# Optimization experiments

Measured on AMD Instinct MI355X. Metric: run time of the kernel, lower is better.

Reference implementation:

```python
import jax, jax.numpy as jnp
import numpy as np

B, T, D = 2, 2048, 1024
H = 16
HD = D // H  # 64


def setup_inputs() -> dict:
    key = jax.random.key(0)
    k1, k2, k3, k4, k5 = jax.random.split(key, 5)
    s = 0.02
    return {
        "x": jax.random.normal(k1, (B, T, D), dtype=jnp.float32),
        "Wqkv": jax.random.normal(k2, (D, 3 * D), dtype=jnp.float32) * s,
        "bqkv": jax.random.normal(k3, (3 * D,), dtype=jnp.float32) * s,
        "Wout": jax.random.normal(k4, (D, D), dtype=jnp.float32) * s,
        "bout": jax.random.normal(k5, (D,), dtype=jnp.float32) * s,
    }


def reference(x, Wqkv, bqkv, Wout, bout):
    b, t, c = x.shape
    qkv = (x @ Wqkv + bqkv).reshape(b, t, 3, H, HD)
    q = jnp.transpose(qkv[:, :, 0], (0, 2, 1, 3))  # [B,H,T,HD]
    k = jnp.transpose(qkv[:, :, 1], (0, 2, 1, 3))
    v = jnp.transpose(qkv[:, :, 2], (0, 2, 1, 3))
    att = jnp.einsum("bhqd,bhkd->bhqk", q, k) * (HD ** -0.5)
    mask = jnp.tril(jnp.ones((t, t), dtype=bool))  # causal, no past kv
    att = jnp.where(mask, att, -jnp.inf)
    att = jax.nn.softmax(att, axis=-1)
    y = jnp.einsum("bhqk,bhkd->bhqd", att, v)
    y = jnp.transpose(y, (0, 2, 1, 3)).reshape(b, t, c)
    return y @ Wout + bout
```

## Files before the change

### kernel.cpp

```cpp
#include <hip/hip_runtime.h>
#include <hip/hip_bf16.h>
#include <math.h>

#define B_  2
#define T_  2048
#define D_  1024
#define H_  16
#define HD_ 64

typedef __attribute__((ext_vector_type(8))) short short8;
typedef __attribute__((ext_vector_type(4))) float f32x4;

#if __has_builtin(__builtin_amdgcn_exp2f)
#define EXP2F __builtin_amdgcn_exp2f
#else
#define EXP2F exp2f
#endif

__device__ __forceinline__ ushort f2bf(float x) {
    unsigned u = __builtin_bit_cast(unsigned, x);
    return (ushort)((u + 0x7FFFu + ((u >> 16) & 1u)) >> 16);
}

__device__ __forceinline__ unsigned pack_bf2_fast(float a, float b) {
    unsigned ua = __builtin_bit_cast(unsigned, a) + 0x8000u;
    unsigned ub = __builtin_bit_cast(unsigned, b) + 0x8000u;
    return (ua >> 16) | (ub & 0xFFFF0000u);
}

__device__ __forceinline__ void load_lds_16B(const ushort* g, ushort* l) {
    __builtin_amdgcn_global_load_lds(
        (const __attribute__((address_space(1))) unsigned*)g,
        (__attribute__((address_space(3))) unsigned*)l, 16, 0, 0);
}

__global__ __launch_bounds__(256)
void cast_x_kernel(const float* __restrict__ x, ushort* __restrict__ xb, int n4)
{
    int i = blockIdx.x * blockDim.x + threadIdx.x;
    for (; i < n4; i += gridDim.x * blockDim.x) {
        float4 v = ((const float4*)x)[i];
        ushort4 o = { f2bf(v.x), f2bf(v.y), f2bf(v.z), f2bf(v.w) };
        ((ushort4*)xb)[i] = o;
    }
}

__global__ __launch_bounds__(256)
void transpose_cast_w(const float* __restrict__ W, ushort* __restrict__ Wt,
                      int K, int M)
{
    __shared__ ushort Ts[64][65];
    const int m0 = blockIdx.x * 64, k0 = blockIdx.y * 64;
    const int tr = threadIdx.x >> 4;
    const int tc = threadIdx.x & 15;
    #pragma unroll
    for (int it = 0; it < 4; it++) {
        int k = tr + it * 16;
        float4 v = *(const float4*)&W[(size_t)(k0 + k) * M + m0 + tc * 4];
        Ts[tc * 4 + 0][k] = f2bf(v.x);
        Ts[tc * 4 + 1][k] = f2bf(v.y);
        Ts[tc * 4 + 2][k] = f2bf(v.z);
        Ts[tc * 4 + 3][k] = f2bf(v.w);
    }
    __syncthreads();
    const int mr = threadIdx.x >> 2;
    const int c4 = threadIdx.x & 3;
    #pragma unroll
    for (int it = 0; it < 4; it++) {
        int kk = c4 * 16 + it * 4;
        ushort4 o = { Ts[mr][kk], Ts[mr][kk + 1], Ts[mr][kk + 2], Ts[mr][kk + 3] };
        *(ushort4*)&Wt[(size_t)(m0 + mr) * K + k0 + kk] = o;
    }
}

template<int MODE>
__global__ __launch_bounds__(256)
void mfma_gemm(const ushort* __restrict__ A, const ushort* __restrict__ Bt,
               const float* __restrict__ bias, float* __restrict__ C,
               ushort* __restrict__ Qg, ushort* __restrict__ Kg,
               ushort* __restrict__ Vtg, int K, int M)
{
    __shared__ __align__(16) ushort lds[16384];
    ushort* Asl = lds;
    ushort* Bsl = lds + 8192;

    const int tid = threadIdx.x;
    const int w  = tid >> 6, L = tid & 63;
    const int lt = L & 15, lq = L >> 4;
    const int wr = w >> 1, wc = w & 1;
    const int m0 = blockIdx.x * 128, n0 = blockIdx.y * 128;
    const int rsub = L >> 3;
    const int pgr  = L & 7;

    f32x4 acc[4][4] = {};

    for (int k0 = 0; k0 < K; k0 += 64) {
        __syncthreads();
        #pragma unroll
        for (int j = 0; j < 4; j++) {
            const int row  = (w * 4 + j) * 8 + rsub;
            const int gran = pgr ^ rsub;
            load_lds_16B(A  + (size_t)(n0 + row) * K + k0 + gran * 8,
                         &Asl[row * 64 + pgr * 8]);
            load_lds_16B(Bt + (size_t)(m0 + row) * K + k0 + gran * 8,
                         &Bsl[row * 64 + pgr * 8]);
        }
        __syncthreads();

        #pragma unroll
        for (int ks = 0; ks < 2; ks++) {
            short8 af[4], bf[4];
            #pragma unroll
            for (int i = 0; i < 4; i++) {
                const int ra = wr * 64 + i * 16 + lt;
                af[i] = *(const short8*)&Asl[ra * 64 + (((ks * 4 + lq) ^ (ra & 7)) * 8)];
                const int rb = wc * 64 + i * 16 + lt;
                bf[i] = *(const short8*)&Bsl[rb * 64 + (((ks * 4 + lq) ^ (rb & 7)) * 8)];
            }
            #pragma unroll
            for (int i = 0; i < 4; i++)
                #pragma unroll
                for (int j = 0; j < 4; j++)
                    acc[i][j] = __builtin_amdgcn_mfma_f32_16x16x32_bf16(af[i], bf[j], acc[i][j], 0, 0, 0);
        }
    }

    if (MODE == 0) {
        #pragma unroll
        for (int j = 0; j < 4; j++) {
            const int m = m0 + wc * 64 + j * 16 + lt;
            const float bv = bias[m];
            #pragma unroll
            for (int i = 0; i < 4; i++) {
                const int n = n0 + wr * 64 + i * 16 + lq * 4;
                #pragma unroll
                for (int r = 0; r < 4; r++)
                    C[(size_t)(n + r) * M + m] = acc[i][j][r] + bv;
            }
        }
    } else {
        const int s = m0 >> 10;
        const float qs = (s == 0) ? 0.18033688011112042f : 1.0f;
        #pragma unroll
        for (int j = 0; j < 4; j++) {
            const int m = m0 + wc * 64 + j * 16 + lt;
            const float bv = bias[m];
            const int h = (m >> 6) & 15, d = m & 63;
            #pragma unroll
            for (int i = 0; i < 4; i++) {
                const int n = n0 + wr * 64 + i * 16 + lq * 4;
                const int b = n >> 11, t = n & 2047;
                if (s < 2) {
                    ushort* dst = (s == 0 ? Qg : Kg);
                    #pragma unroll
                    for (int r = 0; r < 4; r++)
                        dst[((size_t)(b * H_ + h) * T_ + t + r) * HD_ + d] =
                            f2bf((acc[i][j][r] + bv) * qs);
                } else {
                    ushort4 o = { f2bf(acc[i][j][0] + bv), f2bf(acc[i][j][1] + bv),
                                  f2bf(acc[i][j][2] + bv), f2bf(acc[i][j][3] + bv) };
                    *(ushort4*)&Vtg[((size_t)(b * H_ + h) * HD_ + d) * T_ + t] = o;
                }
            }
        }
    }
}

__global__ __launch_bounds__(256, 4)
void attn_mfma(const ushort* __restrict__ Qg, const ushort* __restrict__ Kg,
               const ushort* __restrict__ Vtg, ushort* __restrict__ yb)
{
    const int h = blockIdx.y, b = blockIdx.z;
    const int flip = ((blockIdx.y >> 3) ^ blockIdx.z) & 1;
    const int qb = flip ? blockIdx.x : (31 - blockIdx.x);
    const int tid = threadIdx.x;
    const int w  = tid >> 6, L = tid & 63;
    const int lt = L & 15, lq = L >> 4;
    const int kswz = lt & 7;

    __shared__ __align__(16) ushort Ks [128 * 64];
    __shared__ __align__(16) ushort Vts[64 * 128];
    __shared__ __align__(16) ushort Ps [4][16 * 40];

    const size_t bh = (size_t)(b * H_ + h);
    const ushort* Qbase  = Qg  + bh * T_ * HD_;
    const ushort* Kbase  = Kg  + bh * T_ * HD_;
    const ushort* Vtbase = Vtg + bh * HD_ * T_;

    const int q_glob = qb * 64 + w * 16 + lt;
    const short8 qf0 = *(const short8*)(Qbase + (size_t)q_glob * HD_ + lq * 8);
    const short8 qf1 = *(const short8*)(Qbase + (size_t)q_glob * HD_ + 32 + lq * 8);

    f32x4 acc_o[4] = {};
    float lsum = 0.f;

    const int krow = tid >> 3, kpg = tid & 7;
    const int vrow = tid >> 4, vpg = tid & 15;
    const int nk = (qb + 2) >> 1;

    for (int kb = 0; kb < nk; kb++) {
        __syncthreads();
        #pragma unroll
        for (int rr = 0; rr < 4; rr++) {
            const int row = krow + 32 * rr;
            load_lds_16B(Kbase + (size_t)(kb * 128 + row) * HD_ + (kpg ^ (row & 7)) * 8,
                         &Ks[row * 64 + kpg * 8]);
        }
        #pragma unroll
        for (int rr = 0; rr < 4; rr++) {
            const int d = vrow + 16 * rr;
            load_lds_16B(Vtbase + (size_t)d * T_ + kb * 128 + (vpg ^ (d & 7)) * 8,
                         &Vts[d * 128 + vpg * 8]);
        }
        __syncthreads();

        if (kb < nk - 1) {
            #pragma unroll
            for (int ks = 0; ks < 4; ks++) {
                const int row0 = (2 * ks) * 16 + lt;
                const int row1 = row0 + 16;
                short8 a00 = *(const short8*)&Ks[row0 * 64 + ((lq ^ kswz) * 8)];
                short8 a01 = *(const short8*)&Ks[row0 * 64 + (((4 + lq) ^ kswz) * 8)];
                short8 a10 = *(const short8*)&Ks[row1 * 64 + ((lq ^ kswz) * 8)];
                short8 a11 = *(const short8*)&Ks[row1 * 64 + (((4 + lq) ^ kswz) * 8)];
                f32x4 c0 = {}, c1 = {};
                c0 = __builtin_amdgcn_mfma_f32_16x16x32_bf16(a00, qf0, c0, 0, 0, 0);
                c0 = __builtin_amdgcn_mfma_f32_16x16x32_bf16(a01, qf1, c0, 0, 0, 0);
                c1 = __builtin_amdgcn_mfma_f32_16x16x32_bf16(a10, qf0, c1, 0, 0, 0);
                c1 = __builtin_amdgcn_mfma_f32_16x16x32_bf16(a11, qf1, c1, 0, 0, 0);

                float p0 = EXP2F(c0[0]), p1 = EXP2F(c0[1]);
                float p2 = EXP2F(c0[2]), p3 = EXP2F(c0[3]);
                float p4 = EXP2F(c1[0]), p5 = EXP2F(c1[1]);
                float p6 = EXP2F(c1[2]), p7 = EXP2F(c1[3]);
                lsum += ((p0 + p1) + (p2 + p3)) + ((p4 + p5) + (p6 + p7));
                uint2 pk0 = { pack_bf2_fast(p0, p1), pack_bf2_fast(p2, p3) };
                uint2 pk1 = { pack_bf2_fast(p4, p5), pack_bf2_fast(p6, p7) };
                *(uint2*)&Ps[w][lt * 40 + lq * 4]      = pk0;
                *(uint2*)&Ps[w][lt * 40 + 16 + lq * 4] = pk1;

                short8 pf = *(const short8*)&Ps[w][lt * 40 + lq * 8];

                #pragma unroll
                for (int dt = 0; dt < 4; dt++) {
                    const int vr = dt * 16 + lt;
                    short8 vf = *(const short8*)&Vts[vr * 128 + (((ks * 4 + lq) ^ kswz) * 8)];
                    acc_o[dt] = __builtin_amdgcn_mfma_f32_16x16x32_bf16(pf, vf, acc_o[dt], 0, 0, 0);
                }
            }
        } else {
            const int ksN = (qb & 1) ? 4 : 2;
            const int mk0 = (qb & 1) ? 2 : 0;
            for (int ks = 0; ks < ksN; ks++) {
                const int row0 = (2 * ks) * 16 + lt;
                const int row1 = row0 + 16;
                short8 a00 = *(const short8*)&Ks[row0 * 64 + ((lq ^ kswz) * 8)];
                short8 a01 = *(const short8*)&Ks[row0 * 64 + (((4 + lq) ^ kswz) * 8)];
                short8 a10 = *(const short8*)&Ks[row1 * 64 + ((lq ^ kswz) * 8)];
                short8 a11 = *(const short8*)&Ks[row1 * 64 + (((4 + lq) ^ kswz) * 8)];
                f32x4 c0 = {}, c1 = {};
                c0 = __builtin_amdgcn_mfma_f32_16x16x32_bf16(a00, qf0, c0, 0, 0, 0);
                c0 = __builtin_amdgcn_mfma_f32_16x16x32_bf16(a01, qf1, c0, 0, 0, 0);
                c1 = __builtin_amdgcn_mfma_f32_16x16x32_bf16(a10, qf0, c1, 0, 0, 0);
                c1 = __builtin_amdgcn_mfma_f32_16x16x32_bf16(a11, qf1, c1, 0, 0, 0);

                float p[8];
                #pragma unroll
                for (int r = 0; r < 4; r++) { p[r] = EXP2F(c0[r]); p[4 + r] = EXP2F(c1[r]); }
                if (ks >= mk0) {
                    const int key0 = kb * 128 + (2 * ks) * 16 + lq * 4;
                    #pragma unroll
                    for (int r = 0; r < 4; r++) {
                        if (key0 + r > q_glob)      p[r] = 0.f;
                        if (key0 + 16 + r > q_glob) p[4 + r] = 0.f;
                    }
                }
                lsum += ((p[0] + p[1]) + (p[2] + p[3])) + ((p[4] + p[5]) + (p[6] + p[7]));
                uint2 pk0 = { pack_bf2_fast(p[0], p[1]), pack_bf2_fast(p[2], p[3]) };
                uint2 pk1 = { pack_bf2_fast(p[4], p[5]), pack_bf2_fast(p[6], p[7]) };
                *(uint2*)&Ps[w][lt * 40 + lq * 4]      = pk0;
                *(uint2*)&Ps[w][lt * 40 + 16 + lq * 4] = pk1;

                short8 pf = *(const short8*)&Ps[w][lt * 40 + lq * 8];

                #pragma unroll
                for (int dt = 0; dt < 4; dt++) {
                    const int vr = dt * 16 + lt;
                    short8 vf = *(const short8*)&Vts[vr * 128 + (((ks * 4 + lq) ^ kswz) * 8)];
                    acc_o[dt] = __builtin_amdgcn_mfma_f32_16x16x32_bf16(pf, vf, acc_o[dt], 0, 0, 0);
                }
            }
        }
    }

    lsum += __shfl_xor(lsum, 16, 64);
    lsum += __shfl_xor(lsum, 32, 64);
    const float inv = 1.0f / lsum;

    float linv[4];
    #pragma unroll
    for (int r = 0; r < 4; r++) linv[r] = __shfl(inv, lq * 4 + r, 64);

    ushort* ybase = yb + (size_t)(b * T_ + qb * 64 + w * 16) * D_ + h * HD_;
    #pragma unroll
    for (int r = 0; r < 4; r++)
        #pragma unroll
        for (int dt = 0; dt < 4; dt++)
            ybase[(size_t)(lq * 4 + r) * D_ + dt * 16 + lt] = f2bf(acc_o[dt][r] * linv[r]);
}

extern "C" void kernel_launch(void* const* d_in, const int* in_sizes, int n_in,
                              void* d_out, int out_size, void* d_ws, size_t ws_size,
                              hipStream_t stream)
{
    const float* x    = (const float*)d_in[0];
    const float* Wqkv = (const float*)d_in[1];
    const float* bqkv = (const float*)d_in[2];
    const float* Wout = (const float*)d_in[3];
    const float* bout = (const float*)d_in[4];
    float* out = (float*)d_out;

    char* ws = (char*)d_ws;
    const size_t NT = (size_t)B_ * T_;
    ushort* xb     = (ushort*)ws;
    ushort* Wqkvt  = (ushort*)(ws + NT * D_ * 2);
    ushort* Woutt  = (ushort*)(ws + NT * D_ * 2 + (size_t)3 * D_ * D_ * 2);
    char*   p      = ws + NT * D_ * 2 + (size_t)4 * D_ * D_ * 2;
    const size_t qkv_elems = (size_t)B_ * H_ * T_ * HD_;
    ushort* Qg  = (ushort*)p;
    ushort* Kg  = (ushort*)(p + qkv_elems * 2);
    ushort* Vtg = (ushort*)(p + qkv_elems * 4);
    ushort* yb  = (ushort*)(p + qkv_elems * 6);

    cast_x_kernel<<<1024, 256, 0, stream>>>(x, xb, (int)(NT * D_ / 4));
    transpose_cast_w<<<dim3(3 * D_ / 64, D_ / 64), 256, 0, stream>>>(Wqkv, Wqkvt, D_, 3 * D_);
    transpose_cast_w<<<dim3(D_ / 64, D_ / 64), 256, 0, stream>>>(Wout, Woutt, D_, D_);

    mfma_gemm<1><<<dim3(3 * D_ / 128, NT / 128), 256, 0, stream>>>(
        xb, Wqkvt, bqkv, nullptr, Qg, Kg, Vtg, D_, 3 * D_);

    attn_mfma<<<dim3(32, H_, B_), 256, 0, stream>>>(Qg, Kg, Vtg, yb);

    mfma_gemm<0><<<dim3(D_ / 128, NT / 128), 256, 0, stream>>>(
        yb, Woutt, bout, out, nullptr, nullptr, nullptr, D_, D_);
}
```

Measured before the change: 180.2 us.

## Merge prep kernels into one launch and shrink GEMM tiles to 128x64

The x cast and the two weight transpose-casts are combined into a single prep kernel that dispatches on block index, replacing three launches with one. The bf16 GEMMs now use 128x64 output tiles instead of 128x128, with a smaller LDS footprint and a launch_bounds occupancy hint of 4. This doubles the grid size to improve CU fill and latency hiding. The cost is lower arithmetic intensity per tile and more global reloads of the A operand.

```diff
diff --git a/kernel.cpp b/kernel.cpp
--- a/kernel.cpp
+++ b/kernel.cpp
@@ -35,22 +35,34 @@
 }
 
 __global__ __launch_bounds__(256)
-void cast_x_kernel(const float* __restrict__ x, ushort* __restrict__ xb, int n4)
-{
-    int i = blockIdx.x * blockDim.x + threadIdx.x;
-    for (; i < n4; i += gridDim.x * blockDim.x) {
-        float4 v = ((const float4*)x)[i];
-        ushort4 o = { f2bf(v.x), f2bf(v.y), f2bf(v.z), f2bf(v.w) };
-        ((ushort4*)xb)[i] = o;
-    }
-}
-
-__global__ __launch_bounds__(256)
-void transpose_cast_w(const float* __restrict__ W, ushort* __restrict__ Wt,
-                      int K, int M)
+void prep_kernel(const float* __restrict__ x, ushort* __restrict__ xb,
+                 const float* __restrict__ Wqkv, ushort* __restrict__ Wqkvt,
+                 const float* __restrict__ Wout, ushort* __restrict__ Woutt)
 {
     __shared__ ushort Ts[64][65];
-    const int m0 = blockIdx.x * 64, k0 = blockIdx.y * 64;
+    const int bid = blockIdx.x;
+
+    if (bid < 512) {
+        const int n4 = (B_ * T_ * D_) / 4;
+        for (int i = bid * 256 + threadIdx.x; i < n4; i += 512 * 256) {
+            float4 v = ((const float4*)x)[i];
+            ushort4 o = { f2bf(v.x), f2bf(v.y), f2bf(v.z), f2bf(v.w) };
+            ((ushort4*)xb)[i] = o;
+        }
+        return;
+    }
+
+    const float* W; ushort* Wt; int K, M, m0, k0;
+    if (bid < 1280) {
+        const int t = bid - 512;
+        W = Wqkv; Wt = Wqkvt; K = D_; M = 3 * D_;
+        m0 = (t % 48) * 64; k0 = (t / 48) * 64;
+    } else {
+        const int t = bid - 1280;
+        W = Wout; Wt = Woutt; K = D_; M = D_;
+        m0 = (t % 16) * 64; k0 = (t / 16) * 64;
+    }
+
     const int tr = threadIdx.x >> 4;
     const int tc = threadIdx.x & 15;
     #pragma unroll
@@ -74,13 +86,13 @@
 }
 
 template<int MODE>
-__global__ __launch_bounds__(256)
+__global__ __launch_bounds__(256, 4)
 void mfma_gemm(const ushort* __restrict__ A, const ushort* __restrict__ Bt,
                const float* __restrict__ bias, float* __restrict__ C,
                ushort* __restrict__ Qg, ushort* __restrict__ Kg,
                ushort* __restrict__ Vtg, int K, int M)
 {
-    __shared__ __align__(16) ushort lds[16384];
+    __shared__ __align__(16) ushort lds[8192 + 4096];
     ushort* Asl = lds;
     ushort* Bsl = lds + 8192;
 
@@ -88,11 +100,11 @@
     const int w  = tid >> 6, L = tid & 63;
     const int lt = L & 15, lq = L >> 4;
     const int wr = w >> 1, wc = w & 1;
-    const int m0 = blockIdx.x * 128, n0 = blockIdx.y * 128;
+    const int m0 = blockIdx.x * 64, n0 = blockIdx.y * 128;
     const int rsub = L >> 3;
     const int pgr  = L & 7;
 
-    f32x4 acc[4][4] = {};
+    f32x4 acc[4][2] = {};
 
     for (int k0 = 0; k0 < K; k0 += 64) {
         __syncthreads();
@@ -100,8 +112,13 @@
         for (int j = 0; j < 4; j++) {
             const int row  = (w * 4 + j) * 8 + rsub;
             const int gran = pgr ^ rsub;
-            load_lds_16B(A  + (size_t)(n0 + row) * K + k0 + gran * 8,
+            load_lds_16B(A + (size_t)(n0 + row) * K + k0 + gran * 8,
                          &Asl[row * 64 + pgr * 8]);
+        }
+        #pragma unroll
+        for (int j = 0; j < 2; j++) {
+            const int row  = (w * 2 + j) * 8 + rsub;
+            const int gran = pgr ^ rsub;
             load_lds_16B(Bt + (size_t)(m0 + row) * K + k0 + gran * 8,
                          &Bsl[row * 64 + pgr * 8]);
         }
@@ -109,26 +126,29 @@
 
         #pragma unroll
         for (int ks = 0; ks < 2; ks++) {
-            short8 af[4], bf[4];
+            short8 af[4], bf[2];
             #pragma unroll
             for (int i = 0; i < 4; i++) {
                 const int ra = wr * 64 + i * 16 + lt;
                 af[i] = *(const short8*)&Asl[ra * 64 + (((ks * 4 + lq) ^ (ra & 7)) * 8)];
-                const int rb = wc * 64 + i * 16 + lt;
-                bf[i] = *(const short8*)&Bsl[rb * 64 + (((ks * 4 + lq) ^ (rb & 7)) * 8)];
+            }
+            #pragma unroll
+            for (int j = 0; j < 2; j++) {
+                const int rb = wc * 32 + j * 16 + lt;
+                bf[j] = *(const short8*)&Bsl[rb * 64 + (((ks * 4 + lq) ^ (rb & 7)) * 8)];
             }
             #pragma unroll
             for (int i = 0; i < 4; i++)
                 #pragma unroll
-                for (int j = 0; j < 4; j++)
+                for (int j = 0; j < 2; j++)
                     acc[i][j] = __builtin_amdgcn_mfma_f32_16x16x32_bf16(af[i], bf[j], acc[i][j], 0, 0, 0);
         }
     }
 
     if (MODE == 0) {
         #pragma unroll
-        for (int j = 0; j < 4; j++) {
-            const int m = m0 + wc * 64 + j * 16 + lt;
+        for (int j = 0; j < 2; j++) {
+            const int m = m0 + wc * 32 + j * 16 + lt;
             const float bv = bias[m];
             #pragma unroll
             for (int i = 0; i < 4; i++) {
@@ -142,8 +162,8 @@
         const int s = m0 >> 10;
         const float qs = (s == 0) ? 0.18033688011112042f : 1.0f;
         #pragma unroll
-        for (int j = 0; j < 4; j++) {
-            const int m = m0 + wc * 64 + j * 16 + lt;
+        for (int j = 0; j < 2; j++) {
+            const int m = m0 + wc * 32 + j * 16 + lt;
             const float bv = bias[m];
             const int h = (m >> 6) & 15, d = m & 63;
             #pragma unroll
@@ -332,15 +352,13 @@
     ushort* Vtg = (ushort*)(p + qkv_elems * 4);
     ushort* yb  = (ushort*)(p + qkv_elems * 6);
 
-    cast_x_kernel<<<1024, 256, 0, stream>>>(x, xb, (int)(NT * D_ / 4));
-    transpose_cast_w<<<dim3(3 * D_ / 64, D_ / 64), 256, 0, stream>>>(Wqkv, Wqkvt, D_, 3 * D_);
-    transpose_cast_w<<<dim3(D_ / 64, D_ / 64), 256, 0, stream>>>(Wout, Woutt, D_, D_);
-
-    mfma_gemm<1><<<dim3(3 * D_ / 128, NT / 128), 256, 0, stream>>>(
+    prep_kernel<<<1536, 256, 0, stream>>>(x, xb, Wqkv, Wqkvt, Wout, Woutt);
+
+    mfma_gemm<1><<<dim3(3 * D_ / 64, NT / 128), 256, 0, stream>>>(
         xb, Wqkvt, bqkv, nullptr, Qg, Kg, Vtg, D_, 3 * D_);
 
     attn_mfma<<<dim3(32, H_, B_), 256, 0, stream>>>(Qg, Kg, Vtg, yb);
 
-    mfma_gemm<0><<<dim3(D_ / 128, NT / 128), 256, 0, stream>>>(
+    mfma_gemm<0><<<dim3(D_ / 64, NT / 128), 256, 0, stream>>>(
         yb, Woutt, bout, out, nullptr, nullptr, nullptr, D_, D_);
 }
```

Measured after the change: 176.7 us. -2.0%, faster.
